# Performance work log

Measured on AMD Instinct MI355X. Metric: run time of the kernel, lower is better.

## Reference

```python
import jax, jax.numpy as jnp
import numpy as np

S, B, D, H, L = 512, 64, 1024, 1024, 2


def setup_inputs() -> dict:
    key = jax.random.key(0)
    ks = jax.random.split(key, 10)
    stdv = 1.0 / np.sqrt(H)
    u = lambda k, shp: jax.random.uniform(k, shp, jnp.float32, -stdv, stdv)
    return {
        "x": jax.random.normal(ks[0], (S, B, D), jnp.float32),
        "hx": jnp.zeros((L, B, H), jnp.float32),
        "w_ih_0": u(ks[1], (3 * H, D)),
        "w_hh_0": u(ks[2], (3 * H, H)),
        "b_ih_0": u(ks[3], (3 * H,)),
        "b_hh_0": u(ks[4], (3 * H,)),
        "w_ih_1": u(ks[5], (3 * H, H)),
        "w_hh_1": u(ks[6], (3 * H, H)),
        "b_ih_1": u(ks[7], (3 * H,)),
        "b_hh_1": u(ks[8], (3 * H,)),
    }


def _gru_layer(x, h0, w_ih, w_hh, b_ih, b_hh):
    # Input-to-hidden projection for the whole sequence in one GEMM (same math,
    # x_t does not depend on the recurrence).  (S,B,3H)
    x_lin = jnp.einsum('sbd,gd->sbg', x, w_ih) + b_ih

    def step(h, xl):
        x_r, x_z, x_n = jnp.split(xl, 3, axis=-1)
        h_lin = h @ w_hh.T + b_hh  # (B,3H)
        h_r, h_z, h_n = jnp.split(h_lin, 3, axis=-1)
        r = jax.nn.sigmoid(x_r + h_r)
        z = jax.nn.sigmoid(x_z + h_z)
        n = jnp.tanh(x_n + r * h_n)
        h_new = (1.0 - z) * n + z * h
        return h_new, h_new

    h_last, ys = jax.lax.scan(step, h0, x_lin)
    return ys, h_last


def reference(x, hx, w_ih_0, w_hh_0, b_ih_0, b_hh_0,
              w_ih_1, w_hh_1, b_ih_1, b_hh_1):
    out0, h_f0 = _gru_layer(x, hx[0], w_ih_0, w_hh_0, b_ih_0, b_hh_0)
    out1, h_f1 = _gru_layer(out0, hx[1], w_ih_1, w_hh_1, b_ih_1, b_hh_1)
    hidden = jnp.stack([h_f0, h_f1], axis=0)  # (L,B,H)
    return out1, hidden
```

## Files before the change

### kernel.cpp

```cpp
#include <hip/hip_runtime.h>
#include <stdint.h>


#define SLEN 512
#define HB   65536
#define G3   3072
#define XLSLOT (64 * 64 * 48)

typedef __attribute__((ext_vector_type(8))) short bf16x8;
typedef __attribute__((ext_vector_type(4))) float f32x4;
typedef __attribute__((ext_vector_type(8))) uint16_t u16x8;

__device__ __forceinline__ uint16_t f32_to_bf16(float f) {
  uint32_t u = __float_as_uint(f);
  uint32_t r = u + 0x7FFFu + ((u >> 16) & 1u);
  return (uint16_t)(r >> 16);
}
__device__ __forceinline__ float sigmoid_fast(float x) { return 1.0f / (1.0f + __expf(-x)); }
__device__ __forceinline__ float tanh_fast(float x) { return 1.0f - 2.0f / (1.0f + __expf(2.0f * x)); }
__device__ __forceinline__ void async_cp16(const void* g, void* l) {
  __builtin_amdgcn_global_load_lds((const __attribute__((address_space(1))) void*)g,
                                   (__attribute__((address_space(3))) void*)l, 16, 0, 0);
}
__device__ __forceinline__ void st_u16_llc(uint16_t* p, uint16_t v) {
  __hip_atomic_store(p, v, __ATOMIC_RELAXED, __HIP_MEMORY_SCOPE_AGENT);
}
__device__ __forceinline__ void st_f32_llc(float* p, float v) {
  __hip_atomic_store(p, v, __ATOMIC_RELAXED, __HIP_MEMORY_SCOPE_AGENT);
}
__device__ __forceinline__ void drain_vmem() {
  asm volatile("s_waitcnt vmcnt(0)" ::: "memory");
}
__device__ __forceinline__ int ld_flag(const int* p) {
  return __hip_atomic_load(p, __ATOMIC_RELAXED, __HIP_MEMORY_SCOPE_AGENT);
}
__device__ __forceinline__ void st_flag(int* p, int v) {
  __hip_atomic_store(p, v, __ATOMIC_RELAXED, __HIP_MEMORY_SCOPE_AGENT);
}


__global__ __launch_bounds__(256) void convert_x(const float* __restrict__ src,
                                                 uint16_t* __restrict__ dst) {
  size_t i = ((size_t)blockIdx.x * 256 + threadIdx.x) * 8;
  const float4* s = (const float4*)(src + i);
  float4 a = s[0], b = s[1];
  u16x8 v;
  v[0] = f32_to_bf16(a.x); v[1] = f32_to_bf16(a.y);
  v[2] = f32_to_bf16(a.z); v[3] = f32_to_bf16(a.w);
  v[4] = f32_to_bf16(b.x); v[5] = f32_to_bf16(b.y);
  v[6] = f32_to_bf16(b.z); v[7] = f32_to_bf16(b.w);
  *(u16x8*)(dst + i) = v;
}

__global__ __launch_bounds__(256) void pack_w(const float* __restrict__ src,
                                              uint16_t* __restrict__ dst) {
  int tid = blockIdx.x * 256 + threadIdx.x;
  int tile = tid >> 11, rem = tid & 2047, ks = rem >> 6, lane = rem & 63;
  int row = tile * 16 + (lane & 15);
  int k0 = ks * 32 + (lane >> 4) * 8;
  const float* s = src + (size_t)row * 1024 + k0;
  u16x8 v;
#pragma unroll
  for (int j = 0; j < 8; ++j) v[j] = f32_to_bf16(s[j]);
  *(u16x8*)(dst + (size_t)tid * 8) = v;
}

__global__ __launch_bounds__(256) void init_state(const float* __restrict__ hx,
                                                  uint16_t* __restrict__ h0b,
                                                  uint16_t* __restrict__ h1b,
                                                  int* __restrict__ flags) {
  int i = blockIdx.x * 256 + threadIdx.x;
  h0b[i] = f32_to_bf16(hx[i]);
  h1b[i] = f32_to_bf16(hx[HB + i]);
  if (blockIdx.x < 16) flags[blockIdx.x * 256 + threadIdx.x] = 0;
}

__device__ __forceinline__ void pollA(const int* a0, int t0,
                                      const int* a1, int t1,
                                      const int* a2, int t2) {
  const int BIG = 0x7fffffff;
  int v0 = (t0 > 0) ? ld_flag(a0) : BIG;
  int v1 = (t1 > 0) ? ld_flag(a1) : BIG;
  int v2 = (t2 > 0) ? ld_flag(a2) : BIG;
  int it = 0;
  while (!__all((v0 >= t0) & (v1 >= t1) & (v2 >= t2))) {
    __builtin_amdgcn_s_sleep(1);
    if (v0 < t0) v0 = ld_flag(a0);
    if (v1 < t1) v1 = ld_flag(a1);
    if (v2 < t2) v2 = ld_flag(a2);
    if (++it > (1 << 22)) break;
  }
}


__device__ __forceinline__ void load_a16_sc1(const uint16_t* p, bf16x8* a) {
  asm volatile(
      "global_load_dwordx4 %0, %16, off sc1\n\t"
      "global_load_dwordx4 %1, %16, off offset:64 sc1\n\t"
      "global_load_dwordx4 %2, %16, off offset:128 sc1\n\t"
      "global_load_dwordx4 %3, %16, off offset:192 sc1\n\t"
      "global_load_dwordx4 %4, %16, off offset:256 sc1\n\t"
      "global_load_dwordx4 %5, %16, off offset:320 sc1\n\t"
      "global_load_dwordx4 %6, %16, off offset:384 sc1\n\t"
      "global_load_dwordx4 %7, %16, off offset:448 sc1\n\t"
      "global_load_dwordx4 %8, %16, off offset:512 sc1\n\t"
      "global_load_dwordx4 %9, %16, off offset:576 sc1\n\t"
      "global_load_dwordx4 %10, %16, off offset:640 sc1\n\t"
      "global_load_dwordx4 %11, %16, off offset:704 sc1\n\t"
      "global_load_dwordx4 %12, %16, off offset:768 sc1\n\t"
      "global_load_dwordx4 %13, %16, off offset:832 sc1\n\t"
      "global_load_dwordx4 %14, %16, off offset:896 sc1\n\t"
      "global_load_dwordx4 %15, %16, off offset:960 sc1\n\t"
      "s_waitcnt vmcnt(0)"
      : "=&v"(a[0]), "=&v"(a[1]), "=&v"(a[2]), "=&v"(a[3]),
        "=&v"(a[4]), "=&v"(a[5]), "=&v"(a[6]), "=&v"(a[7]),
        "=&v"(a[8]), "=&v"(a[9]), "=&v"(a[10]), "=&v"(a[11]),
        "=&v"(a[12]), "=&v"(a[13]), "=&v"(a[14]), "=&v"(a[15])
      : "v"(p)
      : "memory");
}

__device__ __forceinline__ void load_a16_xl12_sc1(const uint16_t* p, const float* px,
                                                  bf16x8* a, float* x) {
  asm volatile(
      "global_load_dword %16, %29, off sc1\n\t"
      "global_load_dword %17, %29, off offset:64 sc1\n\t"
      "global_load_dword %18, %29, off offset:128 sc1\n\t"
      "global_load_dword %19, %29, off offset:192 sc1\n\t"
      "global_load_dword %20, %29, off offset:256 sc1\n\t"
      "global_load_dword %21, %29, off offset:320 sc1\n\t"
      "global_load_dword %22, %29, off offset:384 sc1\n\t"
      "global_load_dword %23, %29, off offset:448 sc1\n\t"
      "global_load_dword %24, %29, off offset:512 sc1\n\t"
      "global_load_dword %25, %29, off offset:576 sc1\n\t"
      "global_load_dword %26, %29, off offset:640 sc1\n\t"
      "global_load_dword %27, %29, off offset:704 sc1\n\t"
      "global_load_dwordx4 %0, %28, off sc1\n\t"
      "global_load_dwordx4 %1, %28, off offset:64 sc1\n\t"
      "global_load_dwordx4 %2, %28, off offset:128 sc1\n\t"
      "global_load_dwordx4 %3, %28, off offset:192 sc1\n\t"
      "global_load_dwordx4 %4, %28, off offset:256 sc1\n\t"
      "global_load_dwordx4 %5, %28, off offset:320 sc1\n\t"
      "global_load_dwordx4 %6, %28, off offset:384 sc1\n\t"
      "global_load_dwordx4 %7, %28, off offset:448 sc1\n\t"
      "global_load_dwordx4 %8, %28, off offset:512 sc1\n\t"
      "global_load_dwordx4 %9, %28, off offset:576 sc1\n\t"
      "global_load_dwordx4 %10, %28, off offset:640 sc1\n\t"
      "global_load_dwordx4 %11, %28, off offset:704 sc1\n\t"
      "global_load_dwordx4 %12, %28, off offset:768 sc1\n\t"
      "global_load_dwordx4 %13, %28, off offset:832 sc1\n\t"
      "global_load_dwordx4 %14, %28, off offset:896 sc1\n\t"
      "global_load_dwordx4 %15, %28, off offset:960 sc1\n\t"
      "s_waitcnt vmcnt(0)"
      : "=&v"(a[0]), "=&v"(a[1]), "=&v"(a[2]), "=&v"(a[3]),
        "=&v"(a[4]), "=&v"(a[5]), "=&v"(a[6]), "=&v"(a[7]),
        "=&v"(a[8]), "=&v"(a[9]), "=&v"(a[10]), "=&v"(a[11]),
        "=&v"(a[12]), "=&v"(a[13]), "=&v"(a[14]), "=&v"(a[15]),
        "=&v"(x[0]), "=&v"(x[1]), "=&v"(x[2]), "=&v"(x[3]),
        "=&v"(x[4]), "=&v"(x[5]), "=&v"(x[6]), "=&v"(x[7]),
        "=&v"(x[8]), "=&v"(x[9]), "=&v"(x[10]), "=&v"(x[11])
      : "v"(p), "v"(px)
      : "memory");
}


__device__ __forceinline__ void mfma16(const bf16x8* av, const uint16_t* bbase, int lane,
                                       f32x4& acc0, f32x4& acc1, f32x4& acc2) {
#pragma unroll
  for (int ks = 0; ks < 16; ++ks) {
    const uint16_t* bp = bbase + (size_t)(ks * 64 + lane) * 8;
    bf16x8 b0 = *(const bf16x8*)(bp);
    bf16x8 b1 = *(const bf16x8*)(bp + 16384);
    bf16x8 b2 = *(const bf16x8*)(bp + 32768);
    acc0 = __builtin_amdgcn_mfma_f32_16x16x32_bf16(av[ks], b0, acc0, 0, 0, 0);
    acc1 = __builtin_amdgcn_mfma_f32_16x16x32_bf16(av[ks], b1, acc1, 0, 0, 0);
    acc2 = __builtin_amdgcn_mfma_f32_16x16x32_bf16(av[ks], b2, acc2, 0, 0, 0);
  }
}

__global__ __launch_bounds__(256, 1) void gru_persist(
    const uint16_t* __restrict__ x_bf,
    const uint16_t* __restrict__ wih0, const uint16_t* __restrict__ whh0,
    const uint16_t* __restrict__ wih1, const uint16_t* __restrict__ whh1,
    const float* __restrict__ bih0, const float* __restrict__ bhh0,
    const float* __restrict__ bih1, const float* __restrict__ bhh1,
    const float* __restrict__ hx,
    float* __restrict__ xl0, float* __restrict__ xl1,
    uint16_t* __restrict__ o0r,
    uint16_t* __restrict__ h0b, uint16_t* __restrict__ h1b,
    int* __restrict__ flags,
    float* __restrict__ out) {
  __shared__ uint16_t blds[49152];

  const int task = blockIdx.x >> 6;
  const int slice = blockIdx.x & 63;
  const int tid = threadIdx.x;
  const int lane = tid & 63;
  const int wv = tid >> 6;
  const int r15 = lane & 15;
  const int q = lane >> 4;
  const int c = slice * 16 + r15;
  const int m = 16 * wv + 4 * q;

  int* done0 = flags;
  int* done1 = flags + 1024;
  int* done2 = flags + 2048;
  int* done3 = flags + 3072;
  int* mydone = (task == 0) ? done0 : (task == 1) ? done1 : (task == 2) ? done2 : done3;

  const uint16_t* Bw = (task == 0) ? wih0 : (task == 1) ? whh0 : (task == 2) ? wih1 : whh1;
  const float* bv = (task == 0) ? bih0 : (task == 1) ? bhh0 : (task == 2) ? bih1 : bhh1;
  const float br = bv[c], bz = bv[1024 + c], bn = bv[2048 + c];

  float hreg[4];
  if (task == 1 || task == 3) {
    const int layer = (task == 3);
#pragma unroll
    for (int rg = 0; rg < 4; ++rg)
      hreg[rg] = hx[(size_t)layer * HB + (size_t)(m + rg) * 1024 + c];
  }

#pragma unroll
  for (int i = 0; i < 24; ++i) {
    int s2 = i * 256 + tid;
    int g = s2 >> 11, rem = s2 & 2047, ks = rem >> 6, l = rem & 63;
    const uint16_t* gp = Bw + (size_t)(g * 64 + slice) * 16384 +
                         (size_t)ks * 512 + l * 8;
    async_cp16(gp, blds + (size_t)s2 * 8);
  }
  drain_vmem();
  __syncthreads();

  const int* pw_d1 = done1 + lane * 16;
  const int* pw_d2 = done2 + lane * 16;
  const int* pw_d3 = done3 + lane * 16;
  const int* sl_d0 = done0 + slice * 16;
  const int* sl_d1 = done1 + slice * 16;
  const int* sl_d2 = done2 + slice * 16;
  const int* sl_d3 = done3 + slice * 16;
  const int lo = (lane < 32);

  for (int t = 0; t < SLEN; ++t) {
    if (wv == 0) {
      if (task == 0) {
        pollA(sl_d1, t - 7, flags, 0, flags, 0);
      } else if (task == 1) {
        pollA(sl_d0, t + 1,
              pw_d1, lo ? t : 0,
              pw_d2, t - 7);
      } else if (task == 2) {
        pollA(sl_d3, t - 7,
              pw_d1, lo ? t + 1 : 0,
              flags, 0);
      } else {
        pollA(sl_d2, t + 1,
              pw_d3, lo ? t : 0,
              flags, 0);
      }
    }
    __syncthreads();

    f32x4 acc0 = {0.f, 0.f, 0.f, 0.f}, acc1 = acc0, acc2 = acc0;
    bf16x8 av[16];
    float xv[12];

    if (task == 1 || task == 3) {
      const uint16_t* hb = (task == 1) ? h0b : h1b;
      const float* xlr = (task == 1) ? xl0 : xl1;
      const uint16_t* ap = hb + (size_t)(t & 1) * HB + (size_t)(16 * wv + r15) * 1024 + q * 8;
      const float* xlp = xlr + (size_t)(t & 7) * XLSLOT + (size_t)(slice * 64 + m) * 48 + r15;

      load_a16_xl12_sc1(ap, xlp, av, xv);
      mfma16(av, blds, lane, acc0, acc1, acc2);

      if (wv == 0) pollA(pw_d1 + ((task == 3) ? 2048 : 0), lo ? 0 : t, flags, 0, flags, 0);
      __syncthreads();

      load_a16_sc1(ap + 512, av);
      mfma16(av, blds + 8192, lane, acc0, acc1, acc2);

      uint16_t* hbw = ((task == 1) ? h0b : h1b) + (size_t)((t + 1) & 1) * HB;
      uint16_t* orow = o0r + (size_t)(t & 7) * HB;
#pragma unroll
      for (int rg = 0; rg < 4; ++rg) {
        int mm = m + rg;
        float r = sigmoid_fast(xv[rg * 3 + 0] + acc0[rg] + br);
        float z = sigmoid_fast(xv[rg * 3 + 1] + acc1[rg] + bz);
        float n = tanh_fast(xv[rg * 3 + 2] + r * (acc2[rg] + bn));
        float h = (1.0f - z) * n + z * hreg[rg];
        hreg[rg] = h;
        uint16_t hb16 = f32_to_bf16(h);
        st_u16_llc(hbw + (size_t)mm * 1024 + c, hb16);
        if (task == 1) st_u16_llc(orow + (size_t)mm * 1024 + c, hb16);
      }
      drain_vmem();
      __syncthreads();
      if (tid == 0) st_flag(mydone + slice * 16, t + 1);
      if (task == 3) {
#pragma unroll
        for (int rg = 0; rg < 4; ++rg)
          out[(size_t)t * HB + (size_t)(m + rg) * 1024 + c] = hreg[rg];
      }
    } else {
      if (task == 0) {
        const uint16_t* ap = x_bf + (size_t)t * HB + (size_t)(16 * wv + r15) * 1024 + q * 8;
#pragma unroll
        for (int ks = 0; ks < 16; ++ks) av[ks] = *(const bf16x8*)(ap + ks * 32);
        mfma16(av, blds, lane, acc0, acc1, acc2);
#pragma unroll
        for (int ks = 0; ks < 16; ++ks) av[ks] = *(const bf16x8*)(ap + 512 + ks * 32);
        mfma16(av, blds + 8192, lane, acc0, acc1, acc2);
      } else {
        const uint16_t* ap = o0r + (size_t)(t & 7) * HB + (size_t)(16 * wv + r15) * 1024 + q * 8;
        load_a16_sc1(ap, av);
        mfma16(av, blds, lane, acc0, acc1, acc2);

        if (wv == 0) pollA(pw_d1, lo ? 0 : t + 1, flags, 0, flags, 0);
        __syncthreads();

        load_a16_sc1(ap + 512, av);
        mfma16(av, blds + 8192, lane, acc0, acc1, acc2);
      }
      float* dst = ((task == 0) ? xl0 : xl1) + (size_t)(t & 7) * XLSLOT + (size_t)slice * 64 * 48;
#pragma unroll
      for (int rg = 0; rg < 4; ++rg) {
        int mm = m + rg;
        st_f32_llc(dst + (size_t)mm * 48 + r15,      acc0[rg] + br);
        st_f32_llc(dst + (size_t)mm * 48 + 16 + r15, acc1[rg] + bz);
        st_f32_llc(dst + (size_t)mm * 48 + 32 + r15, acc2[rg] + bn);
      }
      drain_vmem();
      __syncthreads();
      if (tid == 0) st_flag(mydone + slice * 16, t + 1);
    }
  }

  if (task == 1 || task == 3) {
    const int layer = (task == 3);
#pragma unroll
    for (int rg = 0; rg < 4; ++rg)
      out[(size_t)SLEN * HB + (size_t)layer * HB + (size_t)(m + rg) * 1024 + c] = hreg[rg];
  }
}


extern "C" void kernel_launch(void* const* d_in, const int* in_sizes, int n_in,
                              void* d_out, int out_size, void* d_ws, size_t ws_size,
                              hipStream_t stream) {
  (void)in_sizes; (void)n_in; (void)out_size; (void)ws_size;
  const float* x = (const float*)d_in[0];
  const float* hx = (const float*)d_in[1];
  const float* wih0f = (const float*)d_in[2];
  const float* whh0f = (const float*)d_in[3];
  const float* bih0 = (const float*)d_in[4];
  const float* bhh0 = (const float*)d_in[5];
  const float* wih1f = (const float*)d_in[6];
  const float* whh1f = (const float*)d_in[7];
  const float* bih1 = (const float*)d_in[8];
  const float* bhh1 = (const float*)d_in[9];
  float* out = (float*)d_out;

  char* ws = (char*)d_ws;
  uint16_t* x_bf = (uint16_t*)ws; ws += (size_t)SLEN * HB * 2;
  uint16_t* wih0 = (uint16_t*)ws; ws += (size_t)G3 * 1024 * 2;
  uint16_t* whh0 = (uint16_t*)ws; ws += (size_t)G3 * 1024 * 2;
  uint16_t* wih1 = (uint16_t*)ws; ws += (size_t)G3 * 1024 * 2;
  uint16_t* whh1 = (uint16_t*)ws; ws += (size_t)G3 * 1024 * 2;
  float* xl0 = (float*)ws; ws += (size_t)8 * XLSLOT * 4;
  float* xl1 = (float*)ws; ws += (size_t)8 * XLSLOT * 4;
  uint16_t* o0r = (uint16_t*)ws; ws += (size_t)8 * HB * 2;
  uint16_t* h0b = (uint16_t*)ws; ws += (size_t)2 * HB * 2;
  uint16_t* h1b = (uint16_t*)ws; ws += (size_t)2 * HB * 2;
  int* flags = (int*)ws; ws += 16384;

  convert_x<<<16384, 256, 0, stream>>>(x, x_bf);
  pack_w<<<1536, 256, 0, stream>>>(wih0f, wih0);
  pack_w<<<1536, 256, 0, stream>>>(whh0f, whh0);
  pack_w<<<1536, 256, 0, stream>>>(wih1f, wih1);
  pack_w<<<1536, 256, 0, stream>>>(whh1f, whh1);
  init_state<<<256, 256, 0, stream>>>(hx, h0b, h1b, flags);

  const uint16_t* cx = x_bf;
  const uint16_t* cw0 = wih0; const uint16_t* cw1 = whh0;
  const uint16_t* cw2 = wih1; const uint16_t* cw3 = whh1;
  void* args[] = {(void*)&cx, (void*)&cw0, (void*)&cw1, (void*)&cw2, (void*)&cw3,
                  (void*)&bih0, (void*)&bhh0, (void*)&bih1, (void*)&bhh1, (void*)&hx,
                  (void*)&xl0, (void*)&xl1, (void*)&o0r, (void*)&h0b, (void*)&h1b,
                  (void*)&flags, (void*)&out};
  hipError_t e = hipLaunchCooperativeKernel(reinterpret_cast<void*>(gru_persist),
                                            dim3(256), dim3(256), args, 0u, stream);
  if (e != hipSuccess) {
    gru_persist<<<dim3(256), dim3(256), 0, stream>>>(
        x_bf, wih0, whh0, wih1, whh1, bih0, bhh0, bih1, bhh1, hx,
        xl0, xl1, o0r, h0b, h1b, flags, out);
  }
}
```

Baseline: 4.468 ms.

## Repartition persistent GRU into 64 input blocks plus 32-column recurrent blocks

The persistent kernel is repartitioned from 256 blocks (four tasks of 64 slices, 16 columns each) to 160 blocks. Layer-0 input projection keeps 64 blocks, while the recurrent and layer-1 input tasks each use 32 blocks covering 32 columns. Those blocks hold the r and z weights in enlarged LDS and stream the n-gate weights from global memory with register prefetch. The separate o0r ring is dropped: layer-1 input reads layer-0 hidden states from a 4-deep h0 ring, so fewer blocks poll flags each step. The cost is twice the MFMA work per block on the serial recurrent path, extra global traffic for the n-gate weights, and more complex cross-task flag dependencies.

```diff
diff --git a/kernel.cpp b/kernel.cpp
--- a/kernel.cpp
+++ b/kernel.cpp
@@ -27,6 +27,9 @@
 }
 __device__ __forceinline__ void st_f32_llc(float* p, float v) {
   __hip_atomic_store(p, v, __ATOMIC_RELAXED, __HIP_MEMORY_SCOPE_AGENT);
+}
+__device__ __forceinline__ float ld_f32_llc(const float* p) {
+  return __hip_atomic_load(p, __ATOMIC_RELAXED, __HIP_MEMORY_SCOPE_AGENT);
 }
 __device__ __forceinline__ void drain_vmem() {
   asm volatile("s_waitcnt vmcnt(0)" ::: "memory");
@@ -91,7 +94,6 @@
     if (++it > (1 << 22)) break;
   }
 }
-
 
 __device__ __forceinline__ void load_a16_sc1(const uint16_t* p, bf16x8* a) {
   asm volatile(
@@ -120,49 +122,8 @@
       : "memory");
 }
 
-__device__ __forceinline__ void load_a16_xl12_sc1(const uint16_t* p, const float* px,
-                                                  bf16x8* a, float* x) {
-  asm volatile(
-      "global_load_dword %16, %29, off sc1\n\t"
-      "global_load_dword %17, %29, off offset:64 sc1\n\t"
-      "global_load_dword %18, %29, off offset:128 sc1\n\t"
-      "global_load_dword %19, %29, off offset:192 sc1\n\t"
-      "global_load_dword %20, %29, off offset:256 sc1\n\t"
-      "global_load_dword %21, %29, off offset:320 sc1\n\t"
-      "global_load_dword %22, %29, off offset:384 sc1\n\t"
-      "global_load_dword %23, %29, off offset:448 sc1\n\t"
-      "global_load_dword %24, %29, off offset:512 sc1\n\t"
-      "global_load_dword %25, %29, off offset:576 sc1\n\t"
-      "global_load_dword %26, %29, off offset:640 sc1\n\t"
-      "global_load_dword %27, %29, off offset:704 sc1\n\t"
-      "global_load_dwordx4 %0, %28, off sc1\n\t"
-      "global_load_dwordx4 %1, %28, off offset:64 sc1\n\t"
-      "global_load_dwordx4 %2, %28, off offset:128 sc1\n\t"
-      "global_load_dwordx4 %3, %28, off offset:192 sc1\n\t"
-      "global_load_dwordx4 %4, %28, off offset:256 sc1\n\t"
-      "global_load_dwordx4 %5, %28, off offset:320 sc1\n\t"
-      "global_load_dwordx4 %6, %28, off offset:384 sc1\n\t"
-      "global_load_dwordx4 %7, %28, off offset:448 sc1\n\t"
-      "global_load_dwordx4 %8, %28, off offset:512 sc1\n\t"
-      "global_load_dwordx4 %9, %28, off offset:576 sc1\n\t"
-      "global_load_dwordx4 %10, %28, off offset:640 sc1\n\t"
-      "global_load_dwordx4 %11, %28, off offset:704 sc1\n\t"
-      "global_load_dwordx4 %12, %28, off offset:768 sc1\n\t"
-      "global_load_dwordx4 %13, %28, off offset:832 sc1\n\t"
-      "global_load_dwordx4 %14, %28, off offset:896 sc1\n\t"
-      "global_load_dwordx4 %15, %28, off offset:960 sc1\n\t"
-      "s_waitcnt vmcnt(0)"
-      : "=&v"(a[0]), "=&v"(a[1]), "=&v"(a[2]), "=&v"(a[3]),
-        "=&v"(a[4]), "=&v"(a[5]), "=&v"(a[6]), "=&v"(a[7]),
-        "=&v"(a[8]), "=&v"(a[9]), "=&v"(a[10]), "=&v"(a[11]),
-        "=&v"(a[12]), "=&v"(a[13]), "=&v"(a[14]), "=&v"(a[15]),
-        "=&v"(x[0]), "=&v"(x[1]), "=&v"(x[2]), "=&v"(x[3]),
-        "=&v"(x[4]), "=&v"(x[5]), "=&v"(x[6]), "=&v"(x[7]),
-        "=&v"(x[8]), "=&v"(x[9]), "=&v"(x[10]), "=&v"(x[11])
-      : "v"(p), "v"(px)
-      : "memory");
-}
-
+
+#define MFMA_BF16 __builtin_amdgcn_mfma_f32_16x16x32_bf16
 
 __device__ __forceinline__ void mfma16(const bf16x8* av, const uint16_t* bbase, int lane,
                                        f32x4& acc0, f32x4& acc1, f32x4& acc2) {
@@ -172,9 +133,9 @@
     bf16x8 b0 = *(const bf16x8*)(bp);
     bf16x8 b1 = *(const bf16x8*)(bp + 16384);
     bf16x8 b2 = *(const bf16x8*)(bp + 32768);
-    acc0 = __builtin_amdgcn_mfma_f32_16x16x32_bf16(av[ks], b0, acc0, 0, 0, 0);
-    acc1 = __builtin_amdgcn_mfma_f32_16x16x32_bf16(av[ks], b1, acc1, 0, 0, 0);
-    acc2 = __builtin_amdgcn_mfma_f32_16x16x32_bf16(av[ks], b2, acc2, 0, 0, 0);
+    acc0 = MFMA_BF16(av[ks], b0, acc0, 0, 0, 0);
+    acc1 = MFMA_BF16(av[ks], b1, acc1, 0, 0, 0);
+    acc2 = MFMA_BF16(av[ks], b2, acc2, 0, 0, 0);
   }
 }
 
@@ -186,142 +147,69 @@
     const float* __restrict__ bih1, const float* __restrict__ bhh1,
     const float* __restrict__ hx,
     float* __restrict__ xl0, float* __restrict__ xl1,
-    uint16_t* __restrict__ o0r,
     uint16_t* __restrict__ h0b, uint16_t* __restrict__ h1b,
     int* __restrict__ flags,
     float* __restrict__ out) {
-  __shared__ uint16_t blds[49152];
-
-  const int task = blockIdx.x >> 6;
-  const int slice = blockIdx.x & 63;
+  __shared__ uint16_t blds[65536];
+
+  const int b = blockIdx.x;
+  const int task = (b < 64) ? 0 : 1 + ((b - 64) >> 5);
+  const int slice = b & 63;
+  const int w = (b - 64) & 31;
   const int tid = threadIdx.x;
   const int lane = tid & 63;
   const int wv = tid >> 6;
   const int r15 = lane & 15;
   const int q = lane >> 4;
-  const int c = slice * 16 + r15;
   const int m = 16 * wv + 4 * q;
 
   int* done0 = flags;
   int* done1 = flags + 1024;
   int* done2 = flags + 2048;
   int* done3 = flags + 3072;
-  int* mydone = (task == 0) ? done0 : (task == 1) ? done1 : (task == 2) ? done2 : done3;
 
   const uint16_t* Bw = (task == 0) ? wih0 : (task == 1) ? whh0 : (task == 2) ? wih1 : whh1;
   const float* bv = (task == 0) ? bih0 : (task == 1) ? bhh0 : (task == 2) ? bih1 : bhh1;
-  const float br = bv[c], bz = bv[1024 + c], bn = bv[2048 + c];
-
-  float hreg[4];
-  if (task == 1 || task == 3) {
-    const int layer = (task == 3);
-#pragma unroll
-    for (int rg = 0; rg < 4; ++rg)
-      hreg[rg] = hx[(size_t)layer * HB + (size_t)(m + rg) * 1024 + c];
-  }
-
-#pragma unroll
-  for (int i = 0; i < 24; ++i) {
-    int s2 = i * 256 + tid;
-    int g = s2 >> 11, rem = s2 & 2047, ks = rem >> 6, l = rem & 63;
-    const uint16_t* gp = Bw + (size_t)(g * 64 + slice) * 16384 +
-                         (size_t)ks * 512 + l * 8;
-    async_cp16(gp, blds + (size_t)s2 * 8);
+
+  if (task == 0) {
+#pragma unroll
+    for (int i = 0; i < 24; ++i) {
+      int s2 = i * 256 + tid;
+      int g = s2 >> 11, rem = s2 & 2047, ks = rem >> 6, l = rem & 63;
+      const uint16_t* gp = Bw + (size_t)(g * 64 + slice) * 16384 +
+                           (size_t)ks * 512 + l * 8;
+      async_cp16(gp, blds + (size_t)s2 * 8);
+    }
+  } else {
+#pragma unroll
+    for (int i = 0; i < 32; ++i) {
+      int s2 = i * 256 + tid;
+      int g = s2 >> 12, rem = s2 & 4095, ct = rem >> 11, ks = (rem >> 6) & 31, l = rem & 63;
+      const uint16_t* gp = Bw + (size_t)(g * 64 + 2 * w + ct) * 16384 +
+                           (size_t)ks * 512 + l * 8;
+      async_cp16(gp, blds + (size_t)s2 * 8);
+    }
   }
   drain_vmem();
   __syncthreads();
 
-  const int* pw_d1 = done1 + lane * 16;
-  const int* pw_d2 = done2 + lane * 16;
-  const int* pw_d3 = done3 + lane * 16;
-  const int* sl_d0 = done0 + slice * 16;
-  const int* sl_d1 = done1 + slice * 16;
-  const int* sl_d2 = done2 + slice * 16;
-  const int* sl_d3 = done3 + slice * 16;
-  const int lo = (lane < 32);
-
-  for (int t = 0; t < SLEN; ++t) {
-    if (wv == 0) {
-      if (task == 0) {
-        pollA(sl_d1, t - 7, flags, 0, flags, 0);
-      } else if (task == 1) {
-        pollA(sl_d0, t + 1,
-              pw_d1, lo ? t : 0,
-              pw_d2, t - 7);
-      } else if (task == 2) {
-        pollA(sl_d3, t - 7,
-              pw_d1, lo ? t + 1 : 0,
-              flags, 0);
-      } else {
-        pollA(sl_d2, t + 1,
-              pw_d3, lo ? t : 0,
-              flags, 0);
-      }
-    }
-    __syncthreads();
-
-    f32x4 acc0 = {0.f, 0.f, 0.f, 0.f}, acc1 = acc0, acc2 = acc0;
-    bf16x8 av[16];
-    float xv[12];
-
-    if (task == 1 || task == 3) {
-      const uint16_t* hb = (task == 1) ? h0b : h1b;
-      const float* xlr = (task == 1) ? xl0 : xl1;
-      const uint16_t* ap = hb + (size_t)(t & 1) * HB + (size_t)(16 * wv + r15) * 1024 + q * 8;
-      const float* xlp = xlr + (size_t)(t & 7) * XLSLOT + (size_t)(slice * 64 + m) * 48 + r15;
-
-      load_a16_xl12_sc1(ap, xlp, av, xv);
+  if (task == 0) {
+    const int c = slice * 16 + r15;
+    const float br = bv[c], bz = bv[1024 + c], bn = bv[2048 + c];
+    const int* ring = done1 + (slice >> 1) * 16;
+    for (int t = 0; t < SLEN; ++t) {
+      if (wv == 0) pollA(ring, t - 7, flags, 0, flags, 0);
+      __syncthreads();
+      f32x4 acc0 = {0.f, 0.f, 0.f, 0.f}, acc1 = acc0, acc2 = acc0;
+      bf16x8 av[16];
+      const uint16_t* ap = x_bf + (size_t)t * HB + (size_t)(16 * wv + r15) * 1024 + q * 8;
+#pragma unroll
+      for (int ks = 0; ks < 16; ++ks) av[ks] = *(const bf16x8*)(ap + ks * 32);
       mfma16(av, blds, lane, acc0, acc1, acc2);
-
-      if (wv == 0) pollA(pw_d1 + ((task == 3) ? 2048 : 0), lo ? 0 : t, flags, 0, flags, 0);
-      __syncthreads();
-
-      load_a16_sc1(ap + 512, av);
+#pragma unroll
+      for (int ks = 0; ks < 16; ++ks) av[ks] = *(const bf16x8*)(ap + 512 + ks * 32);
       mfma16(av, blds + 8192, lane, acc0, acc1, acc2);
-
-      uint16_t* hbw = ((task == 1) ? h0b : h1b) + (size_t)((t + 1) & 1) * HB;
-      uint16_t* orow = o0r + (size_t)(t & 7) * HB;
-#pragma unroll
-      for (int rg = 0; rg < 4; ++rg) {
-        int mm = m + rg;
-        float r = sigmoid_fast(xv[rg * 3 + 0] + acc0[rg] + br);
-        float z = sigmoid_fast(xv[rg * 3 + 1] + acc1[rg] + bz);
-        float n = tanh_fast(xv[rg * 3 + 2] + r * (acc2[rg] + bn));
-        float h = (1.0f - z) * n + z * hreg[rg];
-        hreg[rg] = h;
-        uint16_t hb16 = f32_to_bf16(h);
-        st_u16_llc(hbw + (size_t)mm * 1024 + c, hb16);
-        if (task == 1) st_u16_llc(orow + (size_t)mm * 1024 + c, hb16);
-      }
-      drain_vmem();
-      __syncthreads();
-      if (tid == 0) st_flag(mydone + slice * 16, t + 1);
-      if (task == 3) {
-#pragma unroll
-        for (int rg = 0; rg < 4; ++rg)
-          out[(size_t)t * HB + (size_t)(m + rg) * 1024 + c] = hreg[rg];
-      }
-    } else {
-      if (task == 0) {
-        const uint16_t* ap = x_bf + (size_t)t * HB + (size_t)(16 * wv + r15) * 1024 + q * 8;
-#pragma unroll
-        for (int ks = 0; ks < 16; ++ks) av[ks] = *(const bf16x8*)(ap + ks * 32);
-        mfma16(av, blds, lane, acc0, acc1, acc2);
-#pragma unroll
-        for (int ks = 0; ks < 16; ++ks) av[ks] = *(const bf16x8*)(ap + 512 + ks * 32);
-        mfma16(av, blds + 8192, lane, acc0, acc1, acc2);
-      } else {
-        const uint16_t* ap = o0r + (size_t)(t & 7) * HB + (size_t)(16 * wv + r15) * 1024 + q * 8;
-        load_a16_sc1(ap, av);
-        mfma16(av, blds, lane, acc0, acc1, acc2);
-
-        if (wv == 0) pollA(pw_d1, lo ? 0 : t + 1, flags, 0, flags, 0);
-        __syncthreads();
-
-        load_a16_sc1(ap + 512, av);
-        mfma16(av, blds + 8192, lane, acc0, acc1, acc2);
-      }
-      float* dst = ((task == 0) ? xl0 : xl1) + (size_t)(t & 7) * XLSLOT + (size_t)slice * 64 * 48;
+      float* dst = xl0 + (size_t)(t & 7) * XLSLOT + (size_t)slice * 64 * 48;
 #pragma unroll
       for (int rg = 0; rg < 4; ++rg) {
         int mm = m + rg;
@@ -331,15 +219,155 @@
       }
       drain_vmem();
       __syncthreads();
-      if (tid == 0) st_flag(mydone + slice * 16, t + 1);
-    }
-  }
-
-  if (task == 1 || task == 3) {
+      if (tid == 0) st_flag(done0 + slice * 16, t + 1);
+    }
+    return;
+  }
+
+  float bR[2], bZ[2], bN[2];
+#pragma unroll
+  for (int ct = 0; ct < 2; ++ct) {
+    int c = w * 32 + ct * 16 + r15;
+    bR[ct] = bv[c]; bZ[ct] = bv[1024 + c]; bN[ct] = bv[2048 + c];
+  }
+
+  const bf16x8* wn0 = (const bf16x8*)(Bw + (size_t)(128 + 2 * w) * 16384);
+  const bf16x8* wn1 = (const bf16x8*)(Bw + (size_t)(129 + 2 * w) * 16384);
+
+  float hreg[4][2];
+  if (task != 2) {
     const int layer = (task == 3);
 #pragma unroll
     for (int rg = 0; rg < 4; ++rg)
-      out[(size_t)SLEN * HB + (size_t)layer * HB + (size_t)(m + rg) * 1024 + c] = hreg[rg];
+#pragma unroll
+      for (int ct = 0; ct < 2; ++ct)
+        hreg[rg][ct] = hx[(size_t)layer * HB + (size_t)(m + rg) * 1024 + w * 32 + ct * 16 + r15];
+  }
+
+  for (int t = 0; t < SLEN; ++t) {
+    if (wv == 0) {
+      if (task == 1) {
+        pollA(done0 + (2 * w + (lane & 1)) * 16, (lane < 2) ? t + 1 : 0,
+              done1 + (lane & 31) * 16, (lane < 32) ? t : 0,
+              done2 + (lane & 31) * 16, (lane < 32) ? t - 3 : 0);
+      } else if (task == 2) {
+        pollA(done1 + (lane & 31) * 16, (lane < 32) ? t + 1 : 0,
+              done3 + w * 16, t - 7,
+              flags, 0);
+      } else {
+        pollA(done2 + w * 16, t + 1,
+              done3 + (lane & 31) * 16, (lane < 32) ? t : 0,
+              flags, 0);
+      }
+    }
+    __syncthreads();
+
+    float xv[3][4][2];
+    if (task != 2) {
+      const float* xlr = (task == 1) ? xl0 : xl1;
+      const float* slot = xlr + (size_t)(t & 7) * XLSLOT;
+#pragma unroll
+      for (int g = 0; g < 3; ++g)
+#pragma unroll
+        for (int rg = 0; rg < 4; ++rg)
+#pragma unroll
+          for (int ct = 0; ct < 2; ++ct)
+            xv[g][rg][ct] = ld_f32_llc(slot + (size_t)((2 * w + ct) * 64 + m + rg) * 48 +
+                                       g * 16 + r15);
+    }
+
+    bf16x8 nf[4][2];
+#pragma unroll
+    for (int p = 0; p < 4; ++p) {
+      nf[p][0] = wn0[p * 64 + lane];
+      nf[p][1] = wn1[p * 64 + lane];
+    }
+
+    const uint16_t* hring = (task == 3) ? h1b : h0b;
+    int slot;
+    if (task == 1) slot = t & 3;
+    else if (task == 2) slot = (t + 1) & 3;
+    else slot = t & 1;
+    const uint16_t* ap = hring + (size_t)slot * HB + (size_t)(16 * wv + r15) * 1024 + q * 8;
+
+    f32x4 aR[2], aZ[2], aN[2];
+#pragma unroll
+    for (int ct = 0; ct < 2; ++ct) { aR[ct] = {0,0,0,0}; aZ[ct] = {0,0,0,0}; aN[ct] = {0,0,0,0}; }
+
+    bf16x8 av[16];
+#pragma unroll
+    for (int half = 0; half < 2; ++half) {
+      load_a16_sc1(ap + half * 512, av);
+#pragma unroll
+      for (int ks = 0; ks < 16; ++ks) {
+        const int K = half * 16 + ks;
+        const uint16_t* lb = blds + (size_t)K * 512 + (size_t)lane * 8;
+        bf16x8 r0 = *(const bf16x8*)(lb);
+        bf16x8 r1 = *(const bf16x8*)(lb + 16384);
+        bf16x8 z0 = *(const bf16x8*)(lb + 32768);
+        bf16x8 z1 = *(const bf16x8*)(lb + 49152);
+        aR[0] = MFMA_BF16(av[ks], r0, aR[0], 0, 0, 0);
+        aR[1] = MFMA_BF16(av[ks], r1, aR[1], 0, 0, 0);
+        aZ[0] = MFMA_BF16(av[ks], z0, aZ[0], 0, 0, 0);
+        aZ[1] = MFMA_BF16(av[ks], z1, aZ[1], 0, 0, 0);
+        aN[0] = MFMA_BF16(av[ks], nf[K & 3][0], aN[0], 0, 0, 0);
+        aN[1] = MFMA_BF16(av[ks], nf[K & 3][1], aN[1], 0, 0, 0);
+        if (K < 28) {
+          nf[K & 3][0] = wn0[(K + 4) * 64 + lane];
+          nf[K & 3][1] = wn1[(K + 4) * 64 + lane];
+        }
+      }
+    }
+
+    if (task == 2) {
+      float* dst = xl1 + (size_t)(t & 7) * XLSLOT;
+#pragma unroll
+      for (int rg = 0; rg < 4; ++rg)
+#pragma unroll
+        for (int ct = 0; ct < 2; ++ct) {
+          float* p = dst + (size_t)((2 * w + ct) * 64 + m + rg) * 48 + r15;
+          st_f32_llc(p,      aR[ct][rg] + bR[ct]);
+          st_f32_llc(p + 16, aZ[ct][rg] + bZ[ct]);
+          st_f32_llc(p + 32, aN[ct][rg] + bN[ct]);
+        }
+      drain_vmem();
+      __syncthreads();
+      if (tid == 0) st_flag(done2 + w * 16, t + 1);
+    } else {
+      uint16_t* hbw = ((task == 1) ? h0b : h1b) +
+                      (size_t)((task == 1) ? ((t + 1) & 3) : ((t + 1) & 1)) * HB;
+#pragma unroll
+      for (int rg = 0; rg < 4; ++rg)
+#pragma unroll
+        for (int ct = 0; ct < 2; ++ct) {
+          float r = sigmoid_fast(xv[0][rg][ct] + aR[ct][rg] + bR[ct]);
+          float z = sigmoid_fast(xv[1][rg][ct] + aZ[ct][rg] + bZ[ct]);
+          float n = tanh_fast(xv[2][rg][ct] + r * (aN[ct][rg] + bN[ct]));
+          float h = (1.0f - z) * n + z * hreg[rg][ct];
+          hreg[rg][ct] = h;
+          st_u16_llc(hbw + (size_t)(m + rg) * 1024 + w * 32 + ct * 16 + r15, f32_to_bf16(h));
+        }
+      drain_vmem();
+      __syncthreads();
+      if (tid == 0) st_flag(((task == 1) ? done1 : done3) + w * 16, t + 1);
+      if (task == 3) {
+#pragma unroll
+        for (int rg = 0; rg < 4; ++rg)
+#pragma unroll
+          for (int ct = 0; ct < 2; ++ct)
+            out[(size_t)t * HB + (size_t)(m + rg) * 1024 + w * 32 + ct * 16 + r15] = hreg[rg][ct];
+      }
+    }
+  }
+
+  if (task != 2) {
+    const int layer = (task == 3);
+#pragma unroll
+    for (int rg = 0; rg < 4; ++rg)
+#pragma unroll
+      for (int ct = 0; ct < 2; ++ct)
+        out[(size_t)SLEN * HB + (size_t)layer * HB + (size_t)(m + rg) * 1024 +
+            w * 32 + ct * 16 + r15] = hreg[rg][ct];
   }
 }
 
@@ -368,8 +396,7 @@
   uint16_t* whh1 = (uint16_t*)ws; ws += (size_t)G3 * 1024 * 2;
   float* xl0 = (float*)ws; ws += (size_t)8 * XLSLOT * 4;
   float* xl1 = (float*)ws; ws += (size_t)8 * XLSLOT * 4;
-  uint16_t* o0r = (uint16_t*)ws; ws += (size_t)8 * HB * 2;
-  uint16_t* h0b = (uint16_t*)ws; ws += (size_t)2 * HB * 2;
+  uint16_t* h0b = (uint16_t*)ws; ws += (size_t)4 * HB * 2;
   uint16_t* h1b = (uint16_t*)ws; ws += (size_t)2 * HB * 2;
   int* flags = (int*)ws; ws += 16384;
 
@@ -385,13 +412,13 @@
   const uint16_t* cw2 = wih1; const uint16_t* cw3 = whh1;
   void* args[] = {(void*)&cx, (void*)&cw0, (void*)&cw1, (void*)&cw2, (void*)&cw3,
                   (void*)&bih0, (void*)&bhh0, (void*)&bih1, (void*)&bhh1, (void*)&hx,
-                  (void*)&xl0, (void*)&xl1, (void*)&o0r, (void*)&h0b, (void*)&h1b,
+                  (void*)&xl0, (void*)&xl1, (void*)&h0b, (void*)&h1b,
                   (void*)&flags, (void*)&out};
   hipError_t e = hipLaunchCooperativeKernel(reinterpret_cast<void*>(gru_persist),
-                                            dim3(256), dim3(256), args, 0u, stream);
+                                            dim3(160), dim3(256), args, 0u, stream);
   if (e != hipSuccess) {
-    gru_persist<<<dim3(256), dim3(256), 0, stream>>>(
+    gru_persist<<<dim3(160), dim3(256), 0, stream>>>(
         x_bf, wih0, whh0, wih1, whh1, bih0, bhh0, bih1, bhh1, hx,
-        xl0, xl1, o0r, h0b, h1b, flags, out);
-  }
-}
+        xl0, xl1, h0b, h1b, flags, out);
+  }
+}
```

Result: slower. 5.866 ms (+31.3%).

## Drop o0r buffer, widen h0 ring, remove mid-step poll, vectorize stores via LDS

Applied to the files above, without the earlier changes.

Removes the separate layer-0 output ring and has layer 1 read h0 directly from a 4-slot h0 ring. The mid-step split poll plus __syncthreads is dropped, so each step waits for all dependencies up front, and the flag dependencies are reworked. Scattered 2-byte and 4-byte atomic stores are staged through LDS and written as 8-byte and 16-byte sc1 stores. The intent is fewer store transactions and less synchronisation per step. The cost is losing the overlap between the first half of the MFMA work and waiting on the remaining producers.

```diff
diff --git a/kernel.cpp b/kernel.cpp
--- a/kernel.cpp
+++ b/kernel.cpp
@@ -22,11 +22,14 @@
   __builtin_amdgcn_global_load_lds((const __attribute__((address_space(1))) void*)g,
                                    (__attribute__((address_space(3))) void*)l, 16, 0, 0);
 }
-__device__ __forceinline__ void st_u16_llc(uint16_t* p, uint16_t v) {
-  __hip_atomic_store(p, v, __ATOMIC_RELAXED, __HIP_MEMORY_SCOPE_AGENT);
-}
 __device__ __forceinline__ void st_f32_llc(float* p, float v) {
   __hip_atomic_store(p, v, __ATOMIC_RELAXED, __HIP_MEMORY_SCOPE_AGENT);
+}
+__device__ __forceinline__ void st_b64_sc1(void* p, uint2 v) {
+  asm volatile("global_store_dwordx2 %0, %1, off sc1" :: "v"(p), "v"(v) : "memory");
+}
+__device__ __forceinline__ void st_b128_sc1(void* p, f32x4 v) {
+  asm volatile("global_store_dwordx4 %0, %1, off sc1" :: "v"(p), "v"(v) : "memory");
 }
 __device__ __forceinline__ void drain_vmem() {
   asm volatile("s_waitcnt vmcnt(0)" ::: "memory");
@@ -164,6 +167,8 @@
 }
 
 
+#define MFMA_BF16 __builtin_amdgcn_mfma_f32_16x16x32_bf16
+
 __device__ __forceinline__ void mfma16(const bf16x8* av, const uint16_t* bbase, int lane,
                                        f32x4& acc0, f32x4& acc1, f32x4& acc2) {
 #pragma unroll
@@ -172,9 +177,9 @@
     bf16x8 b0 = *(const bf16x8*)(bp);
     bf16x8 b1 = *(const bf16x8*)(bp + 16384);
     bf16x8 b2 = *(const bf16x8*)(bp + 32768);
-    acc0 = __builtin_amdgcn_mfma_f32_16x16x32_bf16(av[ks], b0, acc0, 0, 0, 0);
-    acc1 = __builtin_amdgcn_mfma_f32_16x16x32_bf16(av[ks], b1, acc1, 0, 0, 0);
-    acc2 = __builtin_amdgcn_mfma_f32_16x16x32_bf16(av[ks], b2, acc2, 0, 0, 0);
+    acc0 = MFMA_BF16(av[ks], b0, acc0, 0, 0, 0);
+    acc1 = MFMA_BF16(av[ks], b1, acc1, 0, 0, 0);
+    acc2 = MFMA_BF16(av[ks], b2, acc2, 0, 0, 0);
   }
 }
 
@@ -186,11 +191,11 @@
     const float* __restrict__ bih1, const float* __restrict__ bhh1,
     const float* __restrict__ hx,
     float* __restrict__ xl0, float* __restrict__ xl1,
-    uint16_t* __restrict__ o0r,
     uint16_t* __restrict__ h0b, uint16_t* __restrict__ h1b,
     int* __restrict__ flags,
     float* __restrict__ out) {
   __shared__ uint16_t blds[49152];
+  __shared__ float xstage[4][16][48];
 
   const int task = blockIdx.x >> 6;
   const int slice = blockIdx.x & 63;
@@ -231,30 +236,25 @@
   drain_vmem();
   __syncthreads();
 
-  const int* pw_d1 = done1 + lane * 16;
-  const int* pw_d2 = done2 + lane * 16;
-  const int* pw_d3 = done3 + lane * 16;
-  const int* sl_d0 = done0 + slice * 16;
-  const int* sl_d1 = done1 + slice * 16;
-  const int* sl_d2 = done2 + slice * 16;
-  const int* sl_d3 = done3 + slice * 16;
-  const int lo = (lane < 32);
+  const int sr = lane >> 2;
+  const int sc = lane & 3;
 
   for (int t = 0; t < SLEN; ++t) {
     if (wv == 0) {
       if (task == 0) {
-        pollA(sl_d1, t - 7, flags, 0, flags, 0);
+        pollA(done1 + slice * 16, t - 7,
+              flags, 0, flags, 0);
       } else if (task == 1) {
-        pollA(sl_d0, t + 1,
-              pw_d1, lo ? t : 0,
-              pw_d2, t - 7);
+        pollA(done0 + slice * 16, t + 1,
+              done1 + lane * 16, t,
+              done2 + lane * 16, t - 3);
       } else if (task == 2) {
-        pollA(sl_d3, t - 7,
-              pw_d1, lo ? t + 1 : 0,
+        pollA(done1 + lane * 16, t + 1,
+              done3 + slice * 16, t - 7,
               flags, 0);
       } else {
-        pollA(sl_d2, t + 1,
-              pw_d3, lo ? t : 0,
+        pollA(done2 + slice * 16, t + 1,
+              done3 + lane * 16, t,
               flags, 0);
       }
     }
@@ -265,34 +265,31 @@
     float xv[12];
 
     if (task == 1 || task == 3) {
-      const uint16_t* hb = (task == 1) ? h0b : h1b;
       const float* xlr = (task == 1) ? xl0 : xl1;
-      const uint16_t* ap = hb + (size_t)(t & 1) * HB + (size_t)(16 * wv + r15) * 1024 + q * 8;
+      const int rslot = (task == 1) ? (t & 3) : (t & 1);
+      const uint16_t* ap = ((task == 1) ? h0b : h1b) + (size_t)rslot * HB +
+                           (size_t)(16 * wv + r15) * 1024 + q * 8;
       const float* xlp = xlr + (size_t)(t & 7) * XLSLOT + (size_t)(slice * 64 + m) * 48 + r15;
 
       load_a16_xl12_sc1(ap, xlp, av, xv);
       mfma16(av, blds, lane, acc0, acc1, acc2);
-
-      if (wv == 0) pollA(pw_d1 + ((task == 3) ? 2048 : 0), lo ? 0 : t, flags, 0, flags, 0);
-      __syncthreads();
-
       load_a16_sc1(ap + 512, av);
       mfma16(av, blds + 8192, lane, acc0, acc1, acc2);
 
-      uint16_t* hbw = ((task == 1) ? h0b : h1b) + (size_t)((t + 1) & 1) * HB;
-      uint16_t* orow = o0r + (size_t)(t & 7) * HB;
+      const int wslot = (task == 1) ? ((t + 1) & 3) : ((t + 1) & 1);
+      uint16_t* hbw = ((task == 1) ? h0b : h1b) + (size_t)wslot * HB;
+      uint16_t* hstage = (uint16_t*)&xstage[wv][0][0];
 #pragma unroll
       for (int rg = 0; rg < 4; ++rg) {
-        int mm = m + rg;
         float r = sigmoid_fast(xv[rg * 3 + 0] + acc0[rg] + br);
         float z = sigmoid_fast(xv[rg * 3 + 1] + acc1[rg] + bz);
         float n = tanh_fast(xv[rg * 3 + 2] + r * (acc2[rg] + bn));
         float h = (1.0f - z) * n + z * hreg[rg];
         hreg[rg] = h;
-        uint16_t hb16 = f32_to_bf16(h);
-        st_u16_llc(hbw + (size_t)mm * 1024 + c, hb16);
-        if (task == 1) st_u16_llc(orow + (size_t)mm * 1024 + c, hb16);
-      }
+        hstage[(4 * q + rg) * 16 + r15] = f32_to_bf16(h);
+      }
+      uint2 v2 = *(const uint2*)&hstage[sr * 16 + sc * 4];
+      st_b64_sc1(hbw + (size_t)(16 * wv + sr) * 1024 + slice * 16 + sc * 4, v2);
       drain_vmem();
       __syncthreads();
       if (tid == 0) st_flag(mydone + slice * 16, t + 1);
@@ -311,24 +308,25 @@
         for (int ks = 0; ks < 16; ++ks) av[ks] = *(const bf16x8*)(ap + 512 + ks * 32);
         mfma16(av, blds + 8192, lane, acc0, acc1, acc2);
       } else {
-        const uint16_t* ap = o0r + (size_t)(t & 7) * HB + (size_t)(16 * wv + r15) * 1024 + q * 8;
+        const uint16_t* ap = h0b + (size_t)((t + 1) & 3) * HB +
+                             (size_t)(16 * wv + r15) * 1024 + q * 8;
         load_a16_sc1(ap, av);
         mfma16(av, blds, lane, acc0, acc1, acc2);
-
-        if (wv == 0) pollA(pw_d1, lo ? 0 : t + 1, flags, 0, flags, 0);
-        __syncthreads();
-
         load_a16_sc1(ap + 512, av);
         mfma16(av, blds + 8192, lane, acc0, acc1, acc2);
       }
-      float* dst = ((task == 0) ? xl0 : xl1) + (size_t)(t & 7) * XLSLOT + (size_t)slice * 64 * 48;
 #pragma unroll
       for (int rg = 0; rg < 4; ++rg) {
-        int mm = m + rg;
-        st_f32_llc(dst + (size_t)mm * 48 + r15,      acc0[rg] + br);
-        st_f32_llc(dst + (size_t)mm * 48 + 16 + r15, acc1[rg] + bz);
-        st_f32_llc(dst + (size_t)mm * 48 + 32 + r15, acc2[rg] + bn);
-      }
+        xstage[wv][4 * q + rg][r15]      = acc0[rg] + br;
+        xstage[wv][4 * q + rg][16 + r15] = acc1[rg] + bz;
+        xstage[wv][4 * q + rg][32 + r15] = acc2[rg] + bn;
+      }
+      float* dst = ((task == 0) ? xl0 : xl1) + (size_t)(t & 7) * XLSLOT +
+                   (size_t)slice * 64 * 48 + (size_t)(16 * wv + sr) * 48 + sc * 12;
+      const float* srcp = &xstage[wv][sr][sc * 12];
+      st_b128_sc1(dst,     *(const f32x4*)(srcp));
+      st_b128_sc1(dst + 4, *(const f32x4*)(srcp + 4));
+      st_b128_sc1(dst + 8, *(const f32x4*)(srcp + 8));
       drain_vmem();
       __syncthreads();
       if (tid == 0) st_flag(mydone + slice * 16, t + 1);
@@ -368,8 +366,7 @@
   uint16_t* whh1 = (uint16_t*)ws; ws += (size_t)G3 * 1024 * 2;
   float* xl0 = (float*)ws; ws += (size_t)8 * XLSLOT * 4;
   float* xl1 = (float*)ws; ws += (size_t)8 * XLSLOT * 4;
-  uint16_t* o0r = (uint16_t*)ws; ws += (size_t)8 * HB * 2;
-  uint16_t* h0b = (uint16_t*)ws; ws += (size_t)2 * HB * 2;
+  uint16_t* h0b = (uint16_t*)ws; ws += (size_t)4 * HB * 2;
   uint16_t* h1b = (uint16_t*)ws; ws += (size_t)2 * HB * 2;
   int* flags = (int*)ws; ws += 16384;
 
@@ -385,13 +382,13 @@
   const uint16_t* cw2 = wih1; const uint16_t* cw3 = whh1;
   void* args[] = {(void*)&cx, (void*)&cw0, (void*)&cw1, (void*)&cw2, (void*)&cw3,
                   (void*)&bih0, (void*)&bhh0, (void*)&bih1, (void*)&bhh1, (void*)&hx,
-                  (void*)&xl0, (void*)&xl1, (void*)&o0r, (void*)&h0b, (void*)&h1b,
+                  (void*)&xl0, (void*)&xl1, (void*)&h0b, (void*)&h1b,
                   (void*)&flags, (void*)&out};
   hipError_t e = hipLaunchCooperativeKernel(reinterpret_cast<void*>(gru_persist),
                                             dim3(256), dim3(256), args, 0u, stream);
   if (e != hipSuccess) {
     gru_persist<<<dim3(256), dim3(256), 0, stream>>>(
         x_bf, wih0, whh0, wih1, whh1, bih0, bhh0, bih1, bhh1, hx,
-        xl0, xl1, o0r, h0b, h1b, flags, out);
-  }
-}
+        xl0, xl1, h0b, h1b, flags, out);
+  }
+}
```

Measured after the change: 4.808 ms. 7.6% more time.
